# Performance work log

Measured on AMD Instinct MI355X. Metric: run time of the kernel, lower is better.

## Reference

```python
import jax, jax.numpy as jnp
import numpy as np

B, S, D = 8, 1024, 128
EPS = 1e-7
LN_EPS = 1e-3  # keras LayerNormalization default


def setup_inputs() -> dict:
    key = jax.random.key(0)
    ks = jax.random.split(key, 8)
    sd = 1.0 / np.sqrt(D)
    return {
        "x": jax.random.normal(ks[0], (B, S, D), jnp.float32),
        "Wq": jax.random.normal(ks[1], (D, D), jnp.float32) * sd,
        "bq": jnp.zeros((D,), jnp.float32),
        "Wm": jax.random.normal(ks[2], (D, D), jnp.float32) * sd,
        "bm": jnp.zeros((D,), jnp.float32),
        "Ww": jax.random.normal(ks[3], (D, 1), jnp.float32) * sd,
        "bw": jnp.zeros((1,), jnp.float32),
        "Wc": jax.random.normal(ks[4], (D, 1), jnp.float32) * sd,
        "bc": jnp.zeros((1,), jnp.float32),
        "emb_map": jax.random.normal(ks[5], (D, D, D), jnp.float32) * 0.02,
        "gamma": jnp.ones((D,), jnp.float32),
        "beta": jnp.zeros((D,), jnp.float32),
    }


def reference(x, Wq, bq, Wm, bm, Ww, bw, Wc, bc, emb_map, gamma, beta):
    b_, s_, d_ = x.shape
    q = x @ Wq + bq                      # [B,S,D]
    m = jax.nn.sigmoid(x @ Wm + bm)      # [B,S,D]
    w = jax.nn.relu(x @ Ww + bw)         # [B,S,1]
    c = jax.nn.relu(x @ Wc + bc)         # [B,S,1]

    # distances: for query pos i, preceding pos j (j<i) has distance i-j
    idx = jnp.arange(s_)
    dist = (idx[:, None] - idx[None, :]).astype(x.dtype)   # [S,S]
    valid = dist > 0                                       # strict causal
    # cosh positional decay, zero outside causal window -> [B,S,S]
    pe = jnp.where(valid[None], 1.0 / jnp.cosh((dist[None] - c) / (w + EPS)), 0.0)

    # angle between (pe * x_j * m_i + eps) and (q_i + eps), expanded analytically
    qp = q + EPS
    t1 = jnp.einsum('bjd,bid->bij', x, m * qp)             # sum_d x_j m_i q'_i
    s1 = jnp.einsum('bjd,bid->bij', x, m)                  # sum_d x_j m_i
    s2 = jnp.einsum('bjd,bid->bij', x * x, m * m)          # sum_d (x_j m_i)^2
    dot = pe * t1 + EPS * jnp.sum(qp, axis=-1)[:, :, None]
    na = jnp.sqrt(pe * pe * s2 + 2.0 * EPS * pe * s1 + d_ * EPS * EPS)
    nb = jnp.linalg.norm(qp, axis=-1)[:, :, None]
    cos = jnp.where(valid[None], dot / (na * nb), 0.0)
    angle = jnp.where(valid[None], jnp.arccos(cos), 0.0)   # [B,S,S]

    # query_result_i = sum_j pe*angle * x_j  -> [B,S,D]
    qr = jnp.einsum('bij,bjd->bid', pe * angle, x)

    # embedding matrix: current_token (rows) outer query_result (cols),
    # contracted against rank-3 map: out[b,s,d] = sum_{j,k} x[b,s,j] qr[b,s,k] map[d,j,k]
    em = jnp.einsum('bsj,bsk->bsjk', x, qr).reshape(b_, s_, d_ * d_)
    mapped = em @ emb_map.reshape(d_, d_ * d_).T           # [B,S,D]

    res = mapped + x
    mu = jnp.mean(res, axis=-1, keepdims=True)
    var = jnp.var(res, axis=-1, keepdims=True)
    out = (res - mu) / jnp.sqrt(var + LN_EPS) * gamma + beta
    return out  # dropout is identity at inference
```

## Files before the change

### kernel.cpp

```cpp
#include <hip/hip_runtime.h>
#include <hip/hip_bf16.h>
#include <math.h>

#define DD 128
#define SS 1024
#define NROWS 8192
#define EPSF 1e-7f
#define LN_EPSF 1e-3f
#define TCUT 30.0f

typedef __attribute__((ext_vector_type(8))) short bf16x8;
typedef __attribute__((ext_vector_type(4))) float f32x4;
typedef __attribute__((ext_vector_type(16))) float f32x16;

__device__ __forceinline__ void gload_lds16(const void* g, void* l) {
    __builtin_amdgcn_global_load_lds(
        (const __attribute__((address_space(1))) unsigned int*)g,
        (__attribute__((address_space(3))) unsigned int*)l, 16, 0, 0);
}
__device__ __forceinline__ short f2bf(float v) {
    union { __hip_bfloat16 h; short s; } u;
    u.h = __float2bfloat16(v);
    return u.s;
}
__device__ __forceinline__ float bf2f(short s) {
    union { __hip_bfloat16 h; short s; } u; u.s = s;
    return __bfloat162float(u.h);
}

__global__ __launch_bounds__(256) void k0a_emb(const float* __restrict__ emb,
                                               short* __restrict__ embh3) {
    __shared__ float lt[32][128];
    int d = blockIdx.x, js = blockIdx.y, t = threadIdx.x;
    {
        int jl = t >> 3, k0 = (t & 7) * 16;
        const float4* src = (const float4*)(emb + (size_t)d * 16384
                                            + (size_t)(js * 32 + jl) * 128 + k0);
#pragma unroll
        for (int q = 0; q < 4; ++q) *(float4*)&lt[jl][k0 + q * 4] = src[q];
    }
    __syncthreads();
    int ks = t >> 5, l0 = (t & 31) * 2;
    union { bf16x8 v[2]; short s[16]; } ob;
#pragma unroll
    for (int li = 0; li < 2; ++li) {
        int l = l0 + li;
        const float* p = &lt[l & 31][ks * 16 + (l >> 5) * 8];
#pragma unroll
        for (int e = 0; e < 8; ++e) ob.s[li * 8 + e] = f2bf(p[e]);
    }
    short* dst = embh3 + (size_t)(d * 4 + js) * 4096 + (size_t)t * 16;
    *(bf16x8*)dst = ob.v[0];
    *(bf16x8*)(dst + 8) = ob.v[1];
}

__global__ __launch_bounds__(256) void k0w_split(const float* __restrict__ Wq,
        const float* __restrict__ Wm, short* __restrict__ Wfrag) {
    int T = blockIdx.x * 256 + threadIdx.x;
    int e = T & 7, l = (T >> 3) & 63, ks = (T >> 9) & 3, nt = (T >> 11) & 7,
        mat = (T >> 14) & 1;
    int k = ks * 32 + ((l >> 4) & 3) * 8 + e;
    int c = nt * 16 + (l & 15);
    float v = (mat ? Wm : Wq)[k * 128 + c];
    short h = f2bf(v);
    float lo = v - bf2f(h);
    Wfrag[((((size_t)(mat * 2 + 0) * 8 + nt) * 4 + ks) * 64 + l) * 8 + e] = h;
    Wfrag[((((size_t)(mat * 2 + 1) * 8 + nt) * 4 + ks) * 64 + l) * 8 + e] = f2bf(lo);
}

__global__ __launch_bounds__(256) void k0c_xsplit(const float* __restrict__ x,
        const float* __restrict__ Ww, const float* __restrict__ bw,
        const float* __restrict__ Wc, const float* __restrict__ bc,
        short* __restrict__ xh2, short* __restrict__ xl2,
        float* __restrict__ scal) {
    __shared__ float xs[32][129];
    int rb = blockIdx.x, t = threadIdx.x;
    {
        int r = t >> 3, d0 = (t & 7) * 16;
        const float4* src = (const float4*)(x + (size_t)(rb * 32 + r) * 128 + d0);
#pragma unroll
        for (int q = 0; q < 4; ++q) *(float4*)&xs[r][d0 + q * 4] = src[q];
    }
    __syncthreads();
    int ks = (t >> 5) & 3, rf = t >> 7, l0 = (t & 31) * 2;
    union { bf16x8 v[2]; short s[16]; } hb, lb;
#pragma unroll
    for (int li = 0; li < 2; ++li) {
        int l = l0 + li;
        const float* p = &xs[rf * 16 + (l & 15)][ks * 32 + ((l >> 4) & 3) * 8];
#pragma unroll
        for (int e = 0; e < 8; ++e) {
            float v = p[e];
            short h = f2bf(v);
            hb.s[li * 8 + e] = h;
            lb.s[li * 8 + e] = f2bf(v - bf2f(h));
        }
    }
    {
        short* d1 = xh2 + (size_t)rb * 4096 + (size_t)t * 16;
        short* d2 = xl2 + (size_t)rb * 4096 + (size_t)t * 16;
        *(bf16x8*)d1 = hb.v[0]; *(bf16x8*)(d1 + 8) = hb.v[1];
        *(bf16x8*)d2 = lb.v[0]; *(bf16x8*)(d2 + 8) = lb.v[1];
    }
    int rr = t >> 3, seg = t & 7;
    float pw = 0.f, pc = 0.f;
#pragma unroll
    for (int dq = 0; dq < 16; ++dq) {
        float xv = xs[rr][seg * 16 + dq];
        pw = fmaf(xv, Ww[seg * 16 + dq], pw);
        pc = fmaf(xv, Wc[seg * 16 + dq], pc);
    }
    pw += __shfl_xor(pw, 1); pw += __shfl_xor(pw, 2); pw += __shfl_xor(pw, 4);
    pc += __shfl_xor(pc, 1); pc += __shfl_xor(pc, 2); pc += __shfl_xor(pc, 4);
    if (seg == 0) {
        scal[(size_t)(rb * 32 + rr) * 4 + 0] = fmaxf(pw + bw[0], 0.f);
        scal[(size_t)(rb * 32 + rr) * 4 + 1] = fmaxf(pc + bc[0], 0.f);
    }
}

__global__ __launch_bounds__(256) void k1_mfma(
    const short* __restrict__ xh2, const short* __restrict__ xl2,
    const short* __restrict__ Wfrag,
    const float* __restrict__ bq, const float* __restrict__ bm,
    float* __restrict__ mq, float* __restrict__ mo, float* __restrict__ scal)
{
    __shared__ __align__(16) short wl[65536];
    __shared__ float red[32][4][2];
    int t = threadIdx.x, w = t >> 6, l = t & 63;
    int l15 = l & 15, g = l >> 4;
    int row0 = blockIdx.x * 32;
#pragma unroll
    for (int it = 0; it < 32; ++it)
        gload_lds16(Wfrag + (size_t)(it * 256 + t) * 8, wl + (size_t)(it * 256 + w * 64) * 8);
    const short* xb  = xh2 + (size_t)blockIdx.x * 4096;
    const short* xlb = xl2 + (size_t)blockIdx.x * 4096;
    bf16x8 Ah[2][4], Al[2][4];
#pragma unroll
    for (int rf = 0; rf < 2; ++rf)
#pragma unroll
        for (int ks = 0; ks < 4; ++ks) {
            size_t o = ((size_t)(rf * 4 + ks) * 64 + l) * 8;
            Ah[rf][ks] = *(const bf16x8*)(xb + o);
            Al[rf][ks] = *(const bf16x8*)(xlb + o);
        }
    __syncthreads();
    f32x4 accq[2][2] = {}, accm[2][2] = {};
#pragma unroll
    for (int ntp = 0; ntp < 2; ++ntp) {
        int nt = w * 2 + ntp;
#pragma unroll
        for (int ks = 0; ks < 4; ++ks) {
            bf16x8 bhq = *(const bf16x8*)(wl + ((size_t)(0  + nt) * 4 + ks) * 512 + l * 8);
            bf16x8 blq = *(const bf16x8*)(wl + ((size_t)(8  + nt) * 4 + ks) * 512 + l * 8);
            bf16x8 bhm = *(const bf16x8*)(wl + ((size_t)(16 + nt) * 4 + ks) * 512 + l * 8);
            bf16x8 blm = *(const bf16x8*)(wl + ((size_t)(24 + nt) * 4 + ks) * 512 + l * 8);
#pragma unroll
            for (int rf = 0; rf < 2; ++rf) {
                accq[rf][ntp] = __builtin_amdgcn_mfma_f32_16x16x32_bf16(Ah[rf][ks], bhq, accq[rf][ntp], 0, 0, 0);
                accq[rf][ntp] = __builtin_amdgcn_mfma_f32_16x16x32_bf16(Ah[rf][ks], blq, accq[rf][ntp], 0, 0, 0);
                accq[rf][ntp] = __builtin_amdgcn_mfma_f32_16x16x32_bf16(Al[rf][ks], bhq, accq[rf][ntp], 0, 0, 0);
                accm[rf][ntp] = __builtin_amdgcn_mfma_f32_16x16x32_bf16(Ah[rf][ks], bhm, accm[rf][ntp], 0, 0, 0);
                accm[rf][ntp] = __builtin_amdgcn_mfma_f32_16x16x32_bf16(Ah[rf][ks], blm, accm[rf][ntp], 0, 0, 0);
                accm[rf][ntp] = __builtin_amdgcn_mfma_f32_16x16x32_bf16(Al[rf][ks], bhm, accm[rf][ntp], 0, 0, 0);
            }
        }
    }
    float sq1[2][4] = {{0,0,0,0},{0,0,0,0}};
    float sq2[2][4] = {{0,0,0,0},{0,0,0,0}};
#pragma unroll
    for (int ntp = 0; ntp < 2; ++ntp) {
        int c = (w * 2 + ntp) * 16 + l15;
        float bqv = bq[c] + EPSF, bmv = bm[c];
#pragma unroll
        for (int rf = 0; rf < 2; ++rf)
#pragma unroll
            for (int reg = 0; reg < 4; ++reg) {
                int rloc = rf * 16 + g * 4 + reg;
                float qp = accq[rf][ntp][reg] + bqv;
                float mv = 1.0f / (1.0f + expf(-(accm[rf][ntp][reg] + bmv)));
                size_t o = (size_t)(row0 + rloc) * 128 + c;
                mq[o] = mv * qp;
                mo[o] = mv;
                sq1[rf][reg] += qp;
                sq2[rf][reg] += qp * qp;
            }
    }
#pragma unroll
    for (int rf = 0; rf < 2; ++rf)
#pragma unroll
        for (int reg = 0; reg < 4; ++reg) {
            float a = sq1[rf][reg], b = sq2[rf][reg];
            a += __shfl_xor(a, 1); a += __shfl_xor(a, 2);
            a += __shfl_xor(a, 4); a += __shfl_xor(a, 8);
            b += __shfl_xor(b, 1); b += __shfl_xor(b, 2);
            b += __shfl_xor(b, 4); b += __shfl_xor(b, 8);
            if (l15 == 0) {
                red[rf * 16 + g * 4 + reg][w][0] = a;
                red[rf * 16 + g * 4 + reg][w][1] = b;
            }
        }
    __syncthreads();
    if (t < 32) {
        float a = red[t][0][0] + red[t][1][0] + red[t][2][0] + red[t][3][0];
        float b = red[t][0][1] + red[t][1][1] + red[t][2][1] + red[t][3][1];
        scal[(size_t)(row0 + t) * 4 + 2] = a;
        scal[(size_t)(row0 + t) * 4 + 3] = sqrtf(b);
    }
}

__global__ __launch_bounds__(256) void k2_qr(
    const float* __restrict__ x,
    const float* __restrict__ mq, const float* __restrict__ mo,
    const float* __restrict__ scal, short* __restrict__ qrh2)
{
    int row = blockIdx.x;
    int i = row & (SS - 1);
    const float* xb = x + (size_t)(row - i) * DD;
    int t = threadIdx.x, w = t >> 6, l = t & 63;
    int sub = l >> 4, q = l & 15;
    int qo = q * 8;

    float mqv[8], mov[8];
    {
        const float* mp = mq + (size_t)row * DD + qo;
        float4 a = *(const float4*)mp, b = *(const float4*)(mp + 4);
        mqv[0] = a.x; mqv[1] = a.y; mqv[2] = a.z; mqv[3] = a.w;
        mqv[4] = b.x; mqv[5] = b.y; mqv[6] = b.z; mqv[7] = b.w;
        const float* op = mo + (size_t)row * DD + qo;
        float4 c = *(const float4*)op, d = *(const float4*)(op + 4);
        mov[0] = c.x; mov[1] = c.y; mov[2] = c.z; mov[3] = c.w;
        mov[4] = d.x; mov[5] = d.y; mov[6] = d.z; mov[7] = d.w;
    }
    float wv = scal[row * 4 + 0], cv = scal[row * 4 + 1];
    float sumqp = scal[row * 4 + 2], nb = scal[row * 4 + 3];
    float wi = wv + EPSF;
    float dmaxf = cv + TCUT * wi;
    int dmax = (dmaxf >= (float)i) ? i : (int)dmaxf;

    float acc[8] = {0.f, 0.f, 0.f, 0.f, 0.f, 0.f, 0.f, 0.f};
    int nit = (dmax + 15) >> 4;
    int dbase = 1 + w * 4 + sub;
    for (int it = 0; it < nit; ++it) {
        int dist = dbase + it * 16;
        float xv[8];
        if (dist <= dmax) {
            const float* xp = xb + (size_t)(i - dist) * DD + qo;
            float4 a = *(const float4*)xp, b = *(const float4*)(xp + 4);
            xv[0] = a.x; xv[1] = a.y; xv[2] = a.z; xv[3] = a.w;
            xv[4] = b.x; xv[5] = b.y; xv[6] = b.z; xv[7] = b.w;
        } else {
#pragma unroll
            for (int e = 0; e < 8; ++e) xv[e] = 0.f;
        }
        float t1 = 0.f, s1 = 0.f, s2 = 0.f;
#pragma unroll
        for (int e = 0; e < 8; ++e) {
            float xm = xv[e] * mov[e];
            t1 = fmaf(xv[e], mqv[e], t1);
            s1 += xm;
            s2 = fmaf(xm, xm, s2);
        }
#pragma unroll
        for (int off = 1; off < 16; off <<= 1) {
            t1 += __shfl_xor(t1, off);
            s1 += __shfl_xor(s1, off);
            s2 += __shfl_xor(s2, off);
        }
        float tt = ((float)dist - cv) / wi;
        float pe = 1.0f / coshf(tt);
        float dotv = fmaf(pe, t1, EPSF * sumqp);
        float na = sqrtf(fmaf(pe * pe, s2,
                         fmaf(2.0f * EPSF * pe, s1, (float)DD * EPSF * EPSF)));
        float cosv = fminf(1.0f, fmaxf(-1.0f, dotv / (na * nb)));
        float ang = acosf(cosv);
        float wgt = pe * ang;
#pragma unroll
        for (int e = 0; e < 8; ++e) acc[e] = fmaf(wgt, xv[e], acc[e]);
    }
#pragma unroll
    for (int e = 0; e < 8; ++e) {
        acc[e] += __shfl_xor(acc[e], 16);
        acc[e] += __shfl_xor(acc[e], 32);
    }
    __shared__ float sq[4][DD];
    if (l < 16) {
#pragma unroll
        for (int e = 0; e < 8; ++e) sq[w][qo + e] = acc[e];
    }
    __syncthreads();
    if (t < DD) {
        float v = sq[0][t] + sq[1][t] + sq[2][t] + sq[3][t];
        int rbq = row >> 7, rr = row & 127, rt2 = rr >> 5, lp = rr & 31;
        int k = t;
        qrh2[(((size_t)(rbq * 4 + rt2) * 8 + (k >> 4)) * 64
              + (lp + 32 * ((k >> 3) & 1))) * 8 + (k & 7)] = f2bf(v);
    }
}

__global__ __launch_bounds__(512, 2) void k3_gemm(
    const float* __restrict__ x, const short* __restrict__ embh3,
    const short* __restrict__ qrh2, float* __restrict__ part)
{
    __shared__ float xt[32][132];
    __shared__ __align__(16) float sbuf[128][129];
    int t = threadIdx.x, w8 = t >> 6, l = t & 63;
    int l31 = l & 31, hi = l >> 5;
    int rt = w8 & 3, dh = w8 >> 2;
    int rb = blockIdx.x, js = blockIdx.y;

    {
        int r = t & 127, jq = (t >> 7) * 8;
        const float* xp = x + (size_t)(rb * 128 + r) * 128 + js * 32 + jq;
        float4 a = *(const float4*)xp, b = *(const float4*)(xp + 4);
        xt[jq + 0][r] = a.x; xt[jq + 1][r] = a.y;
        xt[jq + 2][r] = a.z; xt[jq + 3][r] = a.w;
        xt[jq + 4][r] = b.x; xt[jq + 5][r] = b.y;
        xt[jq + 6][r] = b.z; xt[jq + 7][r] = b.w;
    }

    bf16x8 Bf[8];
    const short* qb = qrh2 + (size_t)rb * 16384;
#pragma unroll
    for (int ks = 0; ks < 8; ++ks)
        Bf[ks] = *(const bf16x8*)(qb + (size_t)((rt * 8 + ks) * 64 + l) * 8);

    __syncthreads();
    float xv[16];
#pragma unroll
    for (int reg = 0; reg < 16; ++reg) {
        int rowj = (reg & 3) + 8 * (reg >> 2) + 4 * hi;
        xv[reg] = xt[rowj][rt * 32 + l31];
    }

    const short* Abp = embh3 + (size_t)(dh * 256 + js) * 4096 + (size_t)l * 8;

    bf16x8 Aa[8], Ab2[8], Ac[8], Ad2[8];
#pragma unroll
    for (int ks = 0; ks < 8; ++ks) {
        Aa[ks]  = *(const bf16x8*)(Abp + (size_t)ks * 512);
        Ab2[ks] = *(const bf16x8*)(Abp + 16384 + (size_t)ks * 512);
    }

#define COMP(AR, DI)                                                        \
    {                                                                       \
        f32x16 acc;                                                         \
        _Pragma("unroll")                                                   \
        for (int q = 0; q < 16; ++q) acc[q] = 0.f;                          \
        _Pragma("unroll")                                                   \
        for (int ks = 0; ks < 8; ++ks)                                      \
            acc = __builtin_amdgcn_mfma_f32_32x32x16_bf16(AR[ks], Bf[ks],   \
                                                          acc, 0, 0, 0);    \
        float s0 = 0.f, s1 = 0.f, s2 = 0.f, s3 = 0.f;                       \
        _Pragma("unroll")                                                   \
        for (int q = 0; q < 4; ++q) {                                       \
            s0 = fmaf(xv[q * 4 + 0], acc[q * 4 + 0], s0);                   \
            s1 = fmaf(xv[q * 4 + 1], acc[q * 4 + 1], s1);                   \
            s2 = fmaf(xv[q * 4 + 2], acc[q * 4 + 2], s2);                   \
            s3 = fmaf(xv[q * 4 + 3], acc[q * 4 + 3], s3);                   \
        }                                                                   \
        float s = (s0 + s1) + (s2 + s3);                                    \
        s += __shfl_xor(s, 32);                                             \
        if (hi == 0) sbuf[rt * 32 + l31][DI] = s;                           \
    }

#pragma unroll 1
    for (int i = 0; i < 64; i += 4) {
        {
            const short* An = Abp + (size_t)(i + 2) * 16384;
#pragma unroll
            for (int ks = 0; ks < 8; ++ks) {
                Ac[ks]  = *(const bf16x8*)(An + (size_t)ks * 512);
                Ad2[ks] = *(const bf16x8*)(An + 16384 + (size_t)ks * 512);
            }
        }
        COMP(Aa,  dh * 64 + i)
        COMP(Ab2, dh * 64 + i + 1)
        if (i + 4 < 64) {
            const short* An = Abp + (size_t)(i + 4) * 16384;
#pragma unroll
            for (int ks = 0; ks < 8; ++ks) {
                Aa[ks]  = *(const bf16x8*)(An + (size_t)ks * 512);
                Ab2[ks] = *(const bf16x8*)(An + 16384 + (size_t)ks * 512);
            }
        }
        COMP(Ac,  dh * 64 + i + 2)
        COMP(Ad2, dh * 64 + i + 3)
    }
#undef COMP

    __syncthreads();
#pragma unroll
    for (int e = 0; e < 8; ++e) {
        int idx4 = e * 512 + t;
        int r = idx4 >> 5, c4 = (idx4 & 31) * 4;
        *(float4*)(part + (size_t)js * (NROWS * DD)
                   + (size_t)(rb * 128 + r) * 128 + c4)
            = *(const float4*)&sbuf[r][c4];
    }
}

__global__ __launch_bounds__(256) void k4_ln(
    const float* __restrict__ x, const float* __restrict__ part,
    const float* __restrict__ gamma, const float* __restrict__ beta,
    float* __restrict__ out)
{
    int wave = threadIdx.x >> 6, lane = threadIdx.x & 63;
    int row = blockIdx.x * 4 + wave;
    size_t base = (size_t)row * DD;
    float r0 = x[base + lane], r1 = x[base + lane + 64];
#pragma unroll
    for (int p = 0; p < 4; ++p) {
        r0 += part[(size_t)p * NROWS * DD + base + lane];
        r1 += part[(size_t)p * NROWS * DD + base + lane + 64];
    }
    float s = r0 + r1, s2 = r0 * r0 + r1 * r1;
#pragma unroll
    for (int off = 32; off > 0; off >>= 1) {
        s += __shfl_xor(s, off);
        s2 += __shfl_xor(s2, off);
    }
    float mu = s * (1.0f / DD);
    float var = s2 * (1.0f / DD) - mu * mu;
    var = fmaxf(var, 0.0f);
    float rs = rsqrtf(var + LN_EPSF);
    out[base + lane] = (r0 - mu) * rs * gamma[lane] + beta[lane];
    out[base + lane + 64] = (r1 - mu) * rs * gamma[lane + 64] + beta[lane + 64];
}

extern "C" void kernel_launch(void* const* d_in, const int* in_sizes, int n_in,
                              void* d_out, int out_size, void* d_ws, size_t ws_size,
                              hipStream_t stream) {
    const float* x     = (const float*)d_in[0];
    const float* Wq    = (const float*)d_in[1];
    const float* bq    = (const float*)d_in[2];
    const float* Wm    = (const float*)d_in[3];
    const float* bm    = (const float*)d_in[4];
    const float* Ww    = (const float*)d_in[5];
    const float* bw    = (const float*)d_in[6];
    const float* Wc    = (const float*)d_in[7];
    const float* bc    = (const float*)d_in[8];
    const float* emb   = (const float*)d_in[9];
    const float* gamma = (const float*)d_in[10];
    const float* beta  = (const float*)d_in[11];
    float* out = (float*)d_out;
    float* ws  = (float*)d_ws;

    short* embh3 = (short*)ws;
    short* qrh2  = (short*)(ws + 1048576);
    float* scal  = ws + 1572864;
    float* part  = ws + 1605632;
    short* xh2   = (short*)part;
    short* xl2   = (short*)(part + 524288);
    float* mq    = part + 1048576;
    float* mo    = part + 2097152;
    short* Wfrag = (short*)(part + 3145728);

    hipLaunchKernelGGL(k0a_emb,   dim3(128, 4), dim3(256), 0, stream, emb, embh3);
    hipLaunchKernelGGL(k0w_split, dim3(256),    dim3(256), 0, stream, Wq, Wm, Wfrag);
    hipLaunchKernelGGL(k0c_xsplit,dim3(256),    dim3(256), 0, stream,
                       x, Ww, bw, Wc, bc, xh2, xl2, scal);
    hipLaunchKernelGGL(k1_mfma,   dim3(256),    dim3(256), 0, stream,
                       xh2, xl2, Wfrag, bq, bm, mq, mo, scal);
    hipLaunchKernelGGL(k2_qr,     dim3(8192),   dim3(256), 0, stream,
                       x, mq, mo, scal, qrh2);
    hipLaunchKernelGGL(k3_gemm,   dim3(64, 4),  dim3(512), 0, stream,
                       x, embh3, qrh2, part);
    hipLaunchKernelGGL(k4_ln,     dim3(2048),   dim3(256), 0, stream,
                       x, part, gamma, beta, out);
}
```

Before: 96.45 us.

## Split k3 GEMM waves over K-slices and reduce partial sums with LDS atomics

Waves in k3_gemm used to own a 32-row tile and stream the full K dimension of the embedding map. They now each own a quarter of K across all four row tiles, so each loaded A fragment is reused four times and the per-wave A register footprint shrinks. Partial results are summed in shared memory with atomicAdd after the buffer is zeroed, and the output copy now reads scalars instead of a float4. The intent is to cut global load traffic and register pressure, at the price of LDS atomic contention and a reordered reduction.

```diff
diff --git a/kernel.cpp b/kernel.cpp
--- a/kernel.cpp
+++ b/kernel.cpp
@@ -305,8 +305,10 @@
     __shared__ __align__(16) float sbuf[128][129];
     int t = threadIdx.x, w8 = t >> 6, l = t & 63;
     int l31 = l & 31, hi = l >> 5;
-    int rt = w8 & 3, dh = w8 >> 2;
+    int kh = w8 & 3, dh = w8 >> 2;
     int rb = blockIdx.x, js = blockIdx.y;
+
+    for (int idx = t; idx < 128 * 129; idx += 512) ((float*)sbuf)[idx] = 0.f;
 
     {
         int r = t & 127, jq = (t >> 7) * 8;
@@ -318,84 +320,90 @@
         xt[jq + 6][r] = b.z; xt[jq + 7][r] = b.w;
     }
 
-    bf16x8 Bf[8];
+    bf16x8 Bf[4][2];
     const short* qb = qrh2 + (size_t)rb * 16384;
 #pragma unroll
-    for (int ks = 0; ks < 8; ++ks)
-        Bf[ks] = *(const bf16x8*)(qb + (size_t)((rt * 8 + ks) * 64 + l) * 8);
-
-    __syncthreads();
-    float xv[16];
-#pragma unroll
-    for (int reg = 0; reg < 16; ++reg) {
-        int rowj = (reg & 3) + 8 * (reg >> 2) + 4 * hi;
-        xv[reg] = xt[rowj][rt * 32 + l31];
-    }
-
-    const short* Abp = embh3 + (size_t)(dh * 256 + js) * 4096 + (size_t)l * 8;
-
-    bf16x8 Aa[8], Ab2[8], Ac[8], Ad2[8];
-#pragma unroll
-    for (int ks = 0; ks < 8; ++ks) {
-        Aa[ks]  = *(const bf16x8*)(Abp + (size_t)ks * 512);
-        Ab2[ks] = *(const bf16x8*)(Abp + 16384 + (size_t)ks * 512);
-    }
-
-#define COMP(AR, DI)                                                        \
-    {                                                                       \
-        f32x16 acc;                                                         \
-        _Pragma("unroll")                                                   \
-        for (int q = 0; q < 16; ++q) acc[q] = 0.f;                          \
-        _Pragma("unroll")                                                   \
-        for (int ks = 0; ks < 8; ++ks)                                      \
-            acc = __builtin_amdgcn_mfma_f32_32x32x16_bf16(AR[ks], Bf[ks],   \
-                                                          acc, 0, 0, 0);    \
-        float s0 = 0.f, s1 = 0.f, s2 = 0.f, s3 = 0.f;                       \
-        _Pragma("unroll")                                                   \
-        for (int q = 0; q < 4; ++q) {                                       \
-            s0 = fmaf(xv[q * 4 + 0], acc[q * 4 + 0], s0);                   \
-            s1 = fmaf(xv[q * 4 + 1], acc[q * 4 + 1], s1);                   \
-            s2 = fmaf(xv[q * 4 + 2], acc[q * 4 + 2], s2);                   \
-            s3 = fmaf(xv[q * 4 + 3], acc[q * 4 + 3], s3);                   \
-        }                                                                   \
-        float s = (s0 + s1) + (s2 + s3);                                    \
-        s += __shfl_xor(s, 32);                                             \
-        if (hi == 0) sbuf[rt * 32 + l31][DI] = s;                           \
-    }
+    for (int rt = 0; rt < 4; ++rt)
+#pragma unroll
+        for (int p = 0; p < 2; ++p)
+            Bf[rt][p] = *(const bf16x8*)(qb + (size_t)((rt * 8 + 2 * kh + p) * 64 + l) * 8);
+
+    __syncthreads();
+    float xv[4][16];
+#pragma unroll
+    for (int rt = 0; rt < 4; ++rt)
+#pragma unroll
+        for (int reg = 0; reg < 16; ++reg) {
+            int rowj = (reg & 3) + 8 * (reg >> 2) + 4 * hi;
+            xv[rt][reg] = xt[rowj][rt * 32 + l31];
+        }
+
+    const int ibase = kh * 16;
+    const short* Abase = embh3 + (size_t)(dh * 256 + js) * 4096
+                         + (size_t)(2 * kh) * 512 + (size_t)l * 8;
+
+#define LOADA(AR, II)                                                        \
+    {                                                                        \
+        const short* ap_ = Abase + (size_t)((ibase + (II)) & 63) * 16384;    \
+        AR[0] = *(const bf16x8*)(ap_);                                       \
+        AR[1] = *(const bf16x8*)(ap_ + 512);                                 \
+    }
+
+#define COMPD(AR, II)                                                        \
+    {                                                                        \
+        int di_ = dh * 64 + ((ibase + (II)) & 63);                           \
+        _Pragma("unroll")                                                    \
+        for (int rt = 0; rt < 4; ++rt) {                                     \
+            f32x16 acc;                                                      \
+            _Pragma("unroll")                                                \
+            for (int q = 0; q < 16; ++q) acc[q] = 0.f;                       \
+            acc = __builtin_amdgcn_mfma_f32_32x32x16_bf16(AR[0], Bf[rt][0],  \
+                                                          acc, 0, 0, 0);     \
+            acc = __builtin_amdgcn_mfma_f32_32x32x16_bf16(AR[1], Bf[rt][1],  \
+                                                          acc, 0, 0, 0);     \
+            float s0 = 0.f, s1 = 0.f, s2 = 0.f, s3 = 0.f;                    \
+            _Pragma("unroll")                                                \
+            for (int q = 0; q < 4; ++q) {                                    \
+                s0 = fmaf(xv[rt][q * 4 + 0], acc[q * 4 + 0], s0);            \
+                s1 = fmaf(xv[rt][q * 4 + 1], acc[q * 4 + 1], s1);            \
+                s2 = fmaf(xv[rt][q * 4 + 2], acc[q * 4 + 2], s2);            \
+                s3 = fmaf(xv[rt][q * 4 + 3], acc[q * 4 + 3], s3);            \
+            }                                                                \
+            float s = (s0 + s1) + (s2 + s3);                                 \
+            s += __shfl_xor(s, 32);                                          \
+            if (hi == 0) atomicAdd(&sbuf[rt * 32 + l31][di_], s);            \
+        }                                                                    \
+    }
+
+    bf16x8 Aa[2], Ab_[2], Ac_[2], Ad_[2];
+    LOADA(Aa, 0) LOADA(Ab_, 1) LOADA(Ac_, 2) LOADA(Ad_, 3)
 
 #pragma unroll 1
-    for (int i = 0; i < 64; i += 4) {
-        {
-            const short* An = Abp + (size_t)(i + 2) * 16384;
-#pragma unroll
-            for (int ks = 0; ks < 8; ++ks) {
-                Ac[ks]  = *(const bf16x8*)(An + (size_t)ks * 512);
-                Ad2[ks] = *(const bf16x8*)(An + 16384 + (size_t)ks * 512);
-            }
-        }
-        COMP(Aa,  dh * 64 + i)
-        COMP(Ab2, dh * 64 + i + 1)
-        if (i + 4 < 64) {
-            const short* An = Abp + (size_t)(i + 4) * 16384;
-#pragma unroll
-            for (int ks = 0; ks < 8; ++ks) {
-                Aa[ks]  = *(const bf16x8*)(An + (size_t)ks * 512);
-                Ab2[ks] = *(const bf16x8*)(An + 16384 + (size_t)ks * 512);
-            }
-        }
-        COMP(Ac,  dh * 64 + i + 2)
-        COMP(Ad2, dh * 64 + i + 3)
-    }
-#undef COMP
+    for (int ii = 0; ii < 64; ii += 4) {
+        COMPD(Aa, ii + 0)
+        if (ii + 4 < 64) LOADA(Aa, ii + 4)
+        COMPD(Ab_, ii + 1)
+        if (ii + 5 < 64) LOADA(Ab_, ii + 5)
+        COMPD(Ac_, ii + 2)
+        if (ii + 6 < 64) LOADA(Ac_, ii + 6)
+        COMPD(Ad_, ii + 3)
+        if (ii + 7 < 64) LOADA(Ad_, ii + 7)
+    }
+#undef LOADA
+#undef COMPD
 
     __syncthreads();
 #pragma unroll
     for (int e = 0; e < 8; ++e) {
         int idx4 = e * 512 + t;
         int r = idx4 >> 5, c4 = (idx4 & 31) * 4;
+        float4 v;
+        v.x = sbuf[r][c4 + 0];
+        v.y = sbuf[r][c4 + 1];
+        v.z = sbuf[r][c4 + 2];
+        v.w = sbuf[r][c4 + 3];
         *(float4*)(part + (size_t)js * (NROWS * DD)
-                   + (size_t)(rb * 128 + r) * 128 + c4)
-            = *(const float4*)&sbuf[r][c4];
+                   + (size_t)(rb * 128 + r) * 128 + c4) = v;
     }
 }
 
```

New measurement: 152.8 us. +58.5%, slower.
